# Performance work log

Measured on AMD Instinct MI355X. Metric: run time of the kernel, lower is better.

Reference implementation:

```python
import jax, jax.numpy as jnp
import numpy as np

L, B, D = 1024, 4, 1024
E, K, H = 8, 2, 4096


def setup_inputs() -> dict:
    key = jax.random.key(0)
    ks = jax.random.split(key, 12)
    s_g = 1.0 / np.sqrt(D)
    s_h = 1.0 / np.sqrt(H)
    return {
        "inputs": jax.random.normal(ks[0], (L, B, D), jnp.float32),
        "task_param": jax.random.normal(ks[1], (B, D), jnp.float32),
        "gate_img_w": jax.random.normal(ks[2], (D, E), jnp.float32) * s_g,
        "gate_img_b": jnp.zeros((E,), jnp.float32),
        "gate_txt_w": jax.random.normal(ks[3], (D, E), jnp.float32) * s_g,
        "gate_txt_b": jnp.zeros((E,), jnp.float32),
        "task_gate_w": jax.random.normal(ks[4], (D, E), jnp.float32) * s_g,
        "task_gate_b": jnp.zeros((E,), jnp.float32),
        "alpha": jnp.float32(0.5),
        "w1": jax.random.normal(ks[5], (E, D, H), jnp.float32) * s_g,
        "w2": jax.random.normal(ks[6], (E, H, D), jnp.float32) * s_h,
        "is_text": 1,
    }


def reference(inputs, task_param, gate_img_w, gate_img_b, gate_txt_w, gate_txt_b,
              task_gate_w, task_gate_b, alpha, w1, w2, is_text):
    # task gate: (B, E) -> broadcast over L
    task_logits = (task_param @ task_gate_w + task_gate_b)[None]  # (1, B, E)
    if is_text:
        input_logits = inputs @ gate_txt_w + gate_txt_b  # (L, B, E)
    else:
        input_logits = inputs @ gate_img_w + gate_img_b
    gate_logits = (1.0 - alpha) * input_logits + alpha * task_logits  # (L, B, E)

    topk_vals, sel = jax.lax.top_k(gate_logits, K)  # (L, B, K)

    # auxiliary load-balancing loss
    soft = jax.nn.softmax(gate_logits.astype(jnp.float32), axis=-1)
    avg_weight = soft.mean(axis=(0, 1))                       # (E,)
    expert_mask = jax.nn.one_hot(sel, E).sum(axis=2)          # (L, B, E)
    avg_count = expert_mask.mean(axis=(0, 1))                 # (E,)
    l_aux = jnp.mean(avg_weight * avg_count) * E

    # renormalized top-k weights, combined per expert: (L, B, E)
    weights = jax.nn.softmax(topk_vals.astype(jnp.float32), axis=-1).astype(inputs.dtype)
    comb = jnp.sum(jax.nn.one_hot(sel, E, dtype=weights.dtype) * weights[..., None], axis=2)

    # dense per-expert FFN, weighted combine (loop over fixed small E)
    results = jnp.zeros_like(inputs)
    for e in range(E):
        h = jax.nn.gelu(inputs @ w1[e])      # (L, B, H)
        out = h @ w2[e]                      # (L, B, D)
        results = results + comb[..., e:e + 1] * out
    return results, l_aux.astype(jnp.float32)
```

## Files before the change

### kernel.cpp

```cpp
#include <hip/hip_runtime.h>
#include <hip/hip_bf16.h>
#include <math.h>

#define L_ 1024
#define B_ 4
#define D_ 1024
#define E_ 8
#define K_ 2
#define H_ 4096
#define T_ (L_*B_)
#define P_ (T_*K_)
#define PPAD (P_+256)

typedef unsigned short u16;
typedef __attribute__((ext_vector_type(4))) float f32x4;
typedef __attribute__((ext_vector_type(8))) short s16x8;

__device__ __forceinline__ u16 f2bf(float f) {
  uint32_t u = __float_as_uint(f);
  uint32_t r = (u + 0x7FFFu + ((u >> 16) & 1u)) >> 16;
  return (u16)r;
}
__device__ __forceinline__ float gelu_fast(float v) {
  float u = v * (1.0f + 0.044715f * v * v);
  float t = __expf(-1.5957691216057308f * u);
  return v / (1.0f + t);
}

template<int R, int C>
__global__ void convtrans(const float* __restrict__ in, u16* __restrict__ out) {
  __shared__ float tile[64][65];
  int e = blockIdx.z;
  int r0 = blockIdx.y * 64, c0 = blockIdx.x * 64;
  const float* src = in + (size_t)e * R * C;
  u16* dst = out + (size_t)e * R * C;
  int t = threadIdx.x;
  int tr = t >> 4, tc = (t & 15) * 4;
#pragma unroll
  for (int p = 0; p < 4; ++p) {
    int r = tr + p * 16;
    float4 v = *(const float4*)(src + (size_t)(r0 + r) * C + c0 + tc);
    tile[r][tc] = v.x; tile[r][tc+1] = v.y; tile[r][tc+2] = v.z; tile[r][tc+3] = v.w;
  }
  __syncthreads();
#pragma unroll
  for (int p = 0; p < 4; ++p) {
    int c = tr + p * 16;
    ushort4 o;
    o.x = f2bf(tile[tc+0][c]); o.y = f2bf(tile[tc+1][c]);
    o.z = f2bf(tile[tc+2][c]); o.w = f2bf(tile[tc+3][c]);
    *(ushort4*)(dst + (size_t)(c0 + c) * R + r0 + tc) = o;
  }
}

__global__ void gating(const float* __restrict__ x, const float* __restrict__ task_param,
                       const float* __restrict__ gw_img, const float* __restrict__ gb_img,
                       const float* __restrict__ gw_txt, const float* __restrict__ gb_txt,
                       const float* __restrict__ tgw, const float* __restrict__ tgb,
                       const float* __restrict__ alpha_p, const int* __restrict__ is_text_p,
                       float4* __restrict__ sel_w, float* __restrict__ prob_part,
                       int* __restrict__ count_part) {
  __shared__ float wprob[4][8];
  __shared__ int wcnt[4][8];
  int wid = threadIdx.x >> 6, lane = threadIdx.x & 63;
  int t = blockIdx.x * 4 + wid;
  int b = t & (B_ - 1);
  int it = is_text_p[0];
  const float* gw = it ? gw_txt : gw_img;
  const float* gb = it ? gb_txt : gb_img;
  float alpha = alpha_p[0];
  const float* xr = x + (size_t)t * D_;
  const float* tp = task_param + (size_t)b * D_;
  float acc[8] = {0,0,0,0,0,0,0,0};
  float tac[8] = {0,0,0,0,0,0,0,0};
  for (int i = 0; i < D_/64; ++i) {
    int d = i * 64 + lane;
    float xv = xr[d], tv = tp[d];
#pragma unroll
    for (int e = 0; e < 8; ++e) {
      acc[e] += xv * gw[d*8 + e];
      tac[e] += tv * tgw[d*8 + e];
    }
  }
#pragma unroll
  for (int e = 0; e < 8; ++e) {
#pragma unroll
    for (int off = 32; off > 0; off >>= 1) {
      acc[e] += __shfl_xor(acc[e], off);
      tac[e] += __shfl_xor(tac[e], off);
    }
  }
  float lg[8];
#pragma unroll
  for (int e = 0; e < 8; ++e)
    lg[e] = (1.0f - alpha) * (acc[e] + gb[e]) + alpha * (tac[e] + tgb[e]);
  float m = lg[0];
#pragma unroll
  for (int e = 1; e < 8; ++e) m = fmaxf(m, lg[e]);
  float pr[8], ps = 0.f;
#pragma unroll
  for (int e = 0; e < 8; ++e) { pr[e] = expf(lg[e] - m); ps += pr[e]; }
  float inv = 1.0f / ps;
  int i0 = 0; float v0 = lg[0];
#pragma unroll
  for (int e = 1; e < 8; ++e) if (lg[e] > v0) { v0 = lg[e]; i0 = e; }
  int i1 = -1; float v1 = -1e30f;
#pragma unroll
  for (int e = 0; e < 8; ++e) if (e != i0 && lg[e] > v1) { v1 = lg[e]; i1 = e; }
  float ex = expf(v1 - v0);
  float w0 = 1.0f / (1.0f + ex), w1 = ex / (1.0f + ex);
  if (lane == 0) {
    sel_w[t] = make_float4(__int_as_float(i0), __int_as_float(i1), w0, w1);
#pragma unroll
    for (int e = 0; e < 8; ++e) {
      wprob[wid][e] = pr[e] * inv;
      wcnt[wid][e] = (i0 == e) + (i1 == e);
    }
  }
  __syncthreads();
  if (threadIdx.x < 8) {
    int e = threadIdx.x;
    prob_part[blockIdx.x * 8 + e] = wprob[0][e] + wprob[1][e] + wprob[2][e] + wprob[3][e];
    count_part[blockIdx.x * 8 + e] = wcnt[0][e] + wcnt[1][e] + wcnt[2][e] + wcnt[3][e];
  }
}

__global__ void finalize(const float* __restrict__ prob_part, const int* __restrict__ count_part,
                         int* __restrict__ counts, int* __restrict__ offs,
                         int* __restrict__ cursors, float* __restrict__ laux_out) {
  __shared__ float ps_[256];
  __shared__ int cs_[256];
  int t = threadIdx.x;
  int e = t & 7, s = t >> 3;
  float p = 0.f; int c = 0;
  for (int b = s; b < 1024; b += 32) { p += prob_part[b*8 + e]; c += count_part[b*8 + e]; }
  ps_[t] = p; cs_[t] = c;
  __syncthreads();
  for (int st = 16; st > 0; st >>= 1) {
    if (s < st) { ps_[t] += ps_[t + st*8]; cs_[t] += cs_[t + st*8]; }
    __syncthreads();
  }
  if (t == 0) {
    int off = 0; float laux = 0.f;
    for (int ee = 0; ee < 8; ++ee) {
      int cnt = cs_[ee];
      counts[ee] = cnt; offs[ee] = off; cursors[ee] = off; off += cnt;
      laux += (ps_[ee] * (1.0f/4096.0f)) * ((float)cnt * (1.0f/4096.0f));
    }
    *laux_out = laux;
  }
}

__global__ void scatter_gather(const float* __restrict__ x, const float4* __restrict__ sel_w,
                               int* __restrict__ cursors, float* __restrict__ pair_w,
                               int* __restrict__ pair_idx, u16* __restrict__ Xg) {
  int wid = threadIdx.x >> 6, lane = threadIdx.x & 63;
  int t = blockIdx.x * 4 + wid;
  float4 sw = sel_w[t];
  int s0 = __float_as_int(sw.x), s1 = __float_as_int(sw.y);
  int p0 = 0, p1 = 0;
  if (lane == 0) {
    p0 = atomicAdd(&cursors[s0], 1);
    p1 = atomicAdd(&cursors[s1], 1);
  }
  p0 = __shfl(p0, 0); p1 = __shfl(p1, 0);
  if (lane == 0) {
    pair_w[p0] = sw.z; pair_w[p1] = sw.w;
    pair_idx[t*2] = p0; pair_idx[t*2+1] = p1;
  }
  const float* xr = x + (size_t)t * D_;
  u16* d0 = Xg + (size_t)p0 * D_;
  u16* d1 = Xg + (size_t)p1 * D_;
#pragma unroll
  for (int i = 0; i < 4; ++i) {
    int c = i * 256 + lane * 4;
    float4 v = *(const float4*)(xr + c);
    ushort4 o;
    o.x = f2bf(v.x); o.y = f2bf(v.y); o.z = f2bf(v.z); o.w = f2bf(v.w);
    *(ushort4*)(d0 + c) = o;
    *(ushort4*)(d1 + c) = o;
  }
}

template<int EPI, int KDIM, int KLEN, int NOUT, int NPANEL, int KSPLIT, int JSLOTS>
__global__ __launch_bounds__(512, 2)
void gemm256(const u16* __restrict__ Tok, const u16* __restrict__ Wt,
             const int* __restrict__ counts, const int* __restrict__ offs,
             const float* __restrict__ pair_w,
             u16* __restrict__ Hout, float* __restrict__ Cout) {
  int gid = blockIdx.x;
  int e = gid & 7;
  int idx = gid >> 3;
  int panel = idx % NPANEL; idx /= NPANEL;
  int ks = idx % KSPLIT;    idx /= KSPLIT;
  int j0 = idx;
  int ne = counts[e];
  int off = offs[e];
  int kbase = ks * KLEN;
  float* Cpart = Cout + (size_t)ks * P_ * D_;

  __shared__ u16 As[2][16384];
  __shared__ u16 Bs[2][16384];
  int t = threadIdx.x, lane = t & 63, wid = t >> 6;
  int wf = wid & 1, wt = wid >> 1;

  const u16* Wg = Wt + (size_t)e * NOUT * KDIM + (size_t)panel * 256 * KDIM + kbase;

  int rowoff[4]; int ldsoff[4];
#pragma unroll
  for (int i = 0; i < 4; ++i) {
    int slot = i * 512 + t;
    int row = slot >> 3;
    int kk = (slot & 7) ^ (row & 7);
    rowoff[i] = row * KDIM + kk * 8;
    ldsoff[i] = slot * 8;
  }

  int aoff[8][2], boff[4][2];
#pragma unroll
  for (int r = 0; r < 8; ++r) {
    int row = wf * 128 + r * 16 + (lane & 15);
#pragma unroll
    for (int h = 0; h < 2; ++h) {
      int kk = h * 4 + (lane >> 4);
      aoff[r][h] = (row * 8 + (kk ^ (row & 7))) * 8;
    }
  }
#pragma unroll
  for (int f = 0; f < 4; ++f) {
    int row = wt * 64 + f * 16 + (lane & 15);
#pragma unroll
    for (int h = 0; h < 2; ++h) {
      int kk = h * 4 + (lane >> 4);
      boff[f][h] = (row * 8 + (kk ^ (row & 7))) * 8;
    }
  }

  constexpr int NT = KLEN / 64;
  int lr = lane & 15, lg4 = (lane >> 4) * 4;

  for (int bx = j0; bx * 256 < ne; bx += JSLOTS) {
    const u16* Tg = Tok + (size_t)(off + bx * 256) * KDIM + kbase;
    f32x4 acc[8][4] = {};
#pragma unroll
    for (int i = 0; i < 4; ++i) {
      __builtin_amdgcn_global_load_lds(
          (const __attribute__((address_space(1))) void*)(Wg + rowoff[i]),
          (__attribute__((address_space(3))) void*)(&As[0][ldsoff[i]]), 16, 0, 0);
      __builtin_amdgcn_global_load_lds(
          (const __attribute__((address_space(1))) void*)(Tg + rowoff[i]),
          (__attribute__((address_space(3))) void*)(&Bs[0][ldsoff[i]]), 16, 0, 0);
    }
    __syncthreads();
    int cur = 0;
    for (int tt = 0; tt < NT; ++tt) {
      if (tt + 1 < NT) {
        int k0 = (tt + 1) * 64;
        int nb = cur ^ 1;
#pragma unroll
        for (int i = 0; i < 4; ++i) {
          __builtin_amdgcn_global_load_lds(
              (const __attribute__((address_space(1))) void*)(Wg + rowoff[i] + k0),
              (__attribute__((address_space(3))) void*)(&As[nb][ldsoff[i]]), 16, 0, 0);
          __builtin_amdgcn_global_load_lds(
              (const __attribute__((address_space(1))) void*)(Tg + rowoff[i] + k0),
              (__attribute__((address_space(3))) void*)(&Bs[nb][ldsoff[i]]), 16, 0, 0);
        }
      }
      const u16* Ab = &As[cur][0]; const u16* Bb = &Bs[cur][0];
#pragma unroll
      for (int h = 0; h < 2; ++h) {
        s16x8 a[8], b[4];
#pragma unroll
        for (int r = 0; r < 8; ++r) a[r] = *(const s16x8*)(Ab + aoff[r][h]);
#pragma unroll
        for (int f = 0; f < 4; ++f) b[f] = *(const s16x8*)(Bb + boff[f][h]);
#pragma unroll
        for (int r = 0; r < 8; ++r)
#pragma unroll
          for (int f = 0; f < 4; ++f)
            acc[r][f] = __builtin_amdgcn_mfma_f32_16x16x32_bf16(a[r], b[f], acc[r][f], 0, 0, 0);
      }
      __syncthreads();
      cur ^= 1;
    }

#pragma unroll
    for (int f = 0; f < 4; ++f) {
      int tokl = bx * 256 + wt * 64 + f * 16 + lr;
      if (tokl >= ne) continue;
      size_t grow = (size_t)(off + tokl);
      if (EPI == 0) {
#pragma unroll
        for (int r = 0; r < 8; ++r) {
          ushort4 o;
          o.x = f2bf(gelu_fast(acc[r][f][0]));
          o.y = f2bf(gelu_fast(acc[r][f][1]));
          o.z = f2bf(gelu_fast(acc[r][f][2]));
          o.w = f2bf(gelu_fast(acc[r][f][3]));
          *(ushort4*)(Hout + grow * NOUT + panel * 256 + wf * 128 + r * 16 + lg4) = o;
        }
      } else {
        float w = pair_w[grow];
#pragma unroll
        for (int r = 0; r < 8; ++r) {
          float4 o;
          o.x = acc[r][f][0] * w; o.y = acc[r][f][1] * w;
          o.z = acc[r][f][2] * w; o.w = acc[r][f][3] * w;
          *(float4*)(Cpart + grow * NOUT + panel * 256 + wf * 128 + r * 16 + lg4) = o;
        }
      }
    }
  }
}

__global__ void combine(const float* __restrict__ pair_out, const int* __restrict__ pair_idx,
                        float* __restrict__ out) {
  const float* part1 = pair_out + (size_t)P_ * D_;
  int t = blockIdx.x;
  int p0 = pair_idx[t*2], p1 = pair_idx[t*2+1];
  int c = threadIdx.x * 4;
  float4 a0 = *(const float4*)(pair_out + (size_t)p0 * D_ + c);
  float4 a1 = *(const float4*)(part1    + (size_t)p0 * D_ + c);
  float4 b0 = *(const float4*)(pair_out + (size_t)p1 * D_ + c);
  float4 b1 = *(const float4*)(part1    + (size_t)p1 * D_ + c);
  float4 o;
  o.x = (a0.x + a1.x) + (b0.x + b1.x);
  o.y = (a0.y + a1.y) + (b0.y + b1.y);
  o.z = (a0.z + a1.z) + (b0.z + b1.z);
  o.w = (a0.w + a1.w) + (b0.w + b1.w);
  *(float4*)(out + (size_t)t * D_ + c) = o;
}

extern "C" void kernel_launch(void* const* d_in, const int* in_sizes, int n_in,
                              void* d_out, int out_size, void* d_ws, size_t ws_size,
                              hipStream_t stream) {
  const float* inputs      = (const float*)d_in[0];
  const float* task_param  = (const float*)d_in[1];
  const float* gate_img_w  = (const float*)d_in[2];
  const float* gate_img_b  = (const float*)d_in[3];
  const float* gate_txt_w  = (const float*)d_in[4];
  const float* gate_txt_b  = (const float*)d_in[5];
  const float* task_gate_w = (const float*)d_in[6];
  const float* task_gate_b = (const float*)d_in[7];
  const float* alpha       = (const float*)d_in[8];
  const float* w1          = (const float*)d_in[9];
  const float* w2          = (const float*)d_in[10];
  const int*   is_text     = (const int*)d_in[11];
  float* out = (float*)d_out;

  char* ws = (char*)d_ws;
  u16* w1b = (u16*)(ws + 0);
  u16* w2b = (u16*)(ws + 67108864);
  u16* Xg  = (u16*)(ws + 134217728);
  u16* Hb  = (u16*)(ws + 151519232);
  float4* sel_w   = (float4*)(ws + 220725248);
  float* pair_w   = (float*)(ws + 220725248 + 65536);
  int* pair_idx   = (int*)(ws + 220725248 + 98816);
  float* prob_part= (float*)(ws + 220725248 + 131584);
  int* count_part = (int*)(ws + 220725248 + 164352);
  int* counters   = (int*)(ws + 220725248 + 197120);
  float* pair_out = (float*)(ws + 0);

  int* counts  = counters;
  int* offs    = counters + 8;
  int* cursors = counters + 16;

  convtrans<D_, H_><<<dim3(H_/64, D_/64, E_), 256, 0, stream>>>(w1, w1b);
  convtrans<H_, D_><<<dim3(D_/64, H_/64, E_), 256, 0, stream>>>(w2, w2b);
  gating<<<dim3(T_/4), 256, 0, stream>>>(inputs, task_param, gate_img_w, gate_img_b,
      gate_txt_w, gate_txt_b, task_gate_w, task_gate_b, alpha, is_text,
      sel_w, prob_part, count_part);
  finalize<<<dim3(1), 256, 0, stream>>>(prob_part, count_part, counts, offs, cursors,
      out + (size_t)T_ * D_);
  scatter_gather<<<dim3(T_/4), 256, 0, stream>>>(inputs, sel_w, cursors, pair_w, pair_idx, Xg);
  gemm256<0, D_, D_, H_, 16, 1, 2><<<dim3(256), 512, 0, stream>>>(
      Xg, w1b, counts, offs, pair_w, Hb, (float*)nullptr);
  gemm256<1, H_, H_/2, D_, 4, 2, 4><<<dim3(256), 512, 0, stream>>>(
      Hb, w2b, counts, offs, pair_w, (u16*)nullptr, pair_out);
  combine<<<dim3(T_), 256, 0, stream>>>(pair_out, pair_idx, out);
}
```

Baseline: 512.5 us.

## Schedule grouped expert GEMM tiles through an atomic work queue

Replaces the fixed static mapping of blocks to (expert, panel, k-split, token-block) with a persistent work queue. The finalize kernel precomputes per-expert tile counts and prefix offsets, and each block pulls the next tile index with an atomic ticket counter. This is meant to balance uneven expert loads across the 256 blocks, so that no block idles while others loop over heavy experts. In exchange it adds an atomic and a barrier per tile plus a linear search for the expert.

```diff
diff --git a/kernel.cpp b/kernel.cpp
--- a/kernel.cpp
+++ b/kernel.cpp
@@ -26,6 +26,7 @@
   float t = __expf(-1.5957691216057308f * u);
   return v / (1.0f + t);
 }
+
 
 template<int R, int C>
 __global__ void convtrans(const float* __restrict__ in, u16* __restrict__ out) {
@@ -126,8 +127,7 @@
 }
 
 __global__ void finalize(const float* __restrict__ prob_part, const int* __restrict__ count_part,
-                         int* __restrict__ counts, int* __restrict__ offs,
-                         int* __restrict__ cursors, float* __restrict__ laux_out) {
+                         int* __restrict__ meta, float* __restrict__ laux_out) {
   __shared__ float ps_[256];
   __shared__ int cs_[256];
   int t = threadIdx.x;
@@ -142,11 +142,25 @@
   }
   if (t == 0) {
     int off = 0; float laux = 0.f;
+    int u1 = 0, u2 = 0;
     for (int ee = 0; ee < 8; ++ee) {
       int cnt = cs_[ee];
-      counts[ee] = cnt; offs[ee] = off; cursors[ee] = off; off += cnt;
+      meta[ee] = cnt;
+      meta[8 + ee] = off;
+      meta[16 + ee] = off;
+      int nb = (cnt + 255) >> 8;
+      meta[24 + ee] = nb;
+      meta[32 + ee] = u1;
+      meta[41 + ee] = u2;
+      u1 += 16 * nb;
+      u2 += 4 * nb * 2;
+      off += cnt;
       laux += (ps_[ee] * (1.0f/4096.0f)) * ((float)cnt * (1.0f/4096.0f));
     }
+    meta[32 + 8] = u1;
+    meta[41 + 8] = u2;
+    meta[50] = 0;
+    meta[51] = 0;
     *laux_out = laux;
   }
 }
@@ -182,38 +196,30 @@
   }
 }
 
-template<int EPI, int KDIM, int KLEN, int NOUT, int NPANEL, int KSPLIT, int JSLOTS>
+template<int EPI, int KDIM, int KLEN, int NOUT, int NPANEL, int KSPLIT>
 __global__ __launch_bounds__(512, 2)
 void gemm256(const u16* __restrict__ Tok, const u16* __restrict__ Wt,
-             const int* __restrict__ counts, const int* __restrict__ offs,
-             const float* __restrict__ pair_w,
+             int* __restrict__ meta, const float* __restrict__ pair_w,
              u16* __restrict__ Hout, float* __restrict__ Cout) {
-  int gid = blockIdx.x;
-  int e = gid & 7;
-  int idx = gid >> 3;
-  int panel = idx % NPANEL; idx /= NPANEL;
-  int ks = idx % KSPLIT;    idx /= KSPLIT;
-  int j0 = idx;
-  int ne = counts[e];
-  int off = offs[e];
-  int kbase = ks * KLEN;
-  float* Cpart = Cout + (size_t)ks * P_ * D_;
+  const int* offs = meta + 8;
+  const int* nbx  = meta + 24;
+  const int* ub   = (EPI == 0) ? meta + 32 : meta + 41;
+  int* tick       = meta + ((EPI == 0) ? 50 : 51);
 
   __shared__ u16 As[2][16384];
   __shared__ u16 Bs[2][16384];
+  __shared__ int s_u;
   int t = threadIdx.x, lane = t & 63, wid = t >> 6;
   int wf = wid & 1, wt = wid >> 1;
 
-  const u16* Wg = Wt + (size_t)e * NOUT * KDIM + (size_t)panel * 256 * KDIM + kbase;
-
-  int rowoff[4]; int ldsoff[4];
+  int goff[4]; int ldso[4];
 #pragma unroll
   for (int i = 0; i < 4; ++i) {
     int slot = i * 512 + t;
     int row = slot >> 3;
     int kk = (slot & 7) ^ (row & 7);
-    rowoff[i] = row * KDIM + kk * 8;
-    ldsoff[i] = slot * 8;
+    goff[i] = row * KDIM + kk * 8;
+    ldso[i] = slot * 8;
   }
 
   int aoff[8][2], boff[4][2];
@@ -238,33 +244,52 @@
 
   constexpr int NT = KLEN / 64;
   int lr = lane & 15, lg4 = (lane >> 4) * 4;
-
-  for (int bx = j0; bx * 256 < ne; bx += JSLOTS) {
+  int Utot = ub[8];
+
+  for (;;) {
+    if (t == 0) s_u = atomicAdd(tick, 1);
+    __syncthreads();
+    int u = s_u;
+    if (u >= Utot) break;
+    int e = 0;
+    while (u >= ub[e + 1]) ++e;
+    int ul = u - ub[e];
+    int nb = nbx[e];
+    int panel = ul / (nb * KSPLIT);
+    int rem   = ul - panel * (nb * KSPLIT);
+    int bx    = rem / KSPLIT;
+    int ks    = rem - bx * KSPLIT;
+    int ne  = meta[e];
+    int off = offs[e];
+    int kbase = ks * KLEN;
+    float* Cpart = Cout + (size_t)ks * P_ * D_;
+    const u16* Wg = Wt + (size_t)e * NOUT * KDIM + (size_t)panel * 256 * KDIM + kbase;
     const u16* Tg = Tok + (size_t)(off + bx * 256) * KDIM + kbase;
+
     f32x4 acc[8][4] = {};
 #pragma unroll
     for (int i = 0; i < 4; ++i) {
       __builtin_amdgcn_global_load_lds(
-          (const __attribute__((address_space(1))) void*)(Wg + rowoff[i]),
-          (__attribute__((address_space(3))) void*)(&As[0][ldsoff[i]]), 16, 0, 0);
+          (const __attribute__((address_space(1))) void*)(Wg + goff[i]),
+          (__attribute__((address_space(3))) void*)(&As[0][ldso[i]]), 16, 0, 0);
       __builtin_amdgcn_global_load_lds(
-          (const __attribute__((address_space(1))) void*)(Tg + rowoff[i]),
-          (__attribute__((address_space(3))) void*)(&Bs[0][ldsoff[i]]), 16, 0, 0);
+          (const __attribute__((address_space(1))) void*)(Tg + goff[i]),
+          (__attribute__((address_space(3))) void*)(&Bs[0][ldso[i]]), 16, 0, 0);
     }
     __syncthreads();
     int cur = 0;
     for (int tt = 0; tt < NT; ++tt) {
       if (tt + 1 < NT) {
         int k0 = (tt + 1) * 64;
-        int nb = cur ^ 1;
+        int nbuf = cur ^ 1;
 #pragma unroll
         for (int i = 0; i < 4; ++i) {
           __builtin_amdgcn_global_load_lds(
-              (const __attribute__((address_space(1))) void*)(Wg + rowoff[i] + k0),
-              (__attribute__((address_space(3))) void*)(&As[nb][ldsoff[i]]), 16, 0, 0);
+              (const __attribute__((address_space(1))) void*)(Wg + goff[i] + k0),
+              (__attribute__((address_space(3))) void*)(&As[nbuf][ldso[i]]), 16, 0, 0);
           __builtin_amdgcn_global_load_lds(
-              (const __attribute__((address_space(1))) void*)(Tg + rowoff[i] + k0),
-              (__attribute__((address_space(3))) void*)(&Bs[nb][ldsoff[i]]), 16, 0, 0);
+              (const __attribute__((address_space(1))) void*)(Tg + goff[i] + k0),
+              (__attribute__((address_space(3))) void*)(&Bs[nbuf][ldso[i]]), 16, 0, 0);
         }
       }
       const u16* Ab = &As[cur][0]; const u16* Bb = &Bs[cur][0];
@@ -359,24 +384,20 @@
   int* pair_idx   = (int*)(ws + 220725248 + 98816);
   float* prob_part= (float*)(ws + 220725248 + 131584);
   int* count_part = (int*)(ws + 220725248 + 164352);
-  int* counters   = (int*)(ws + 220725248 + 197120);
+  int* meta       = (int*)(ws + 220725248 + 197120);
   float* pair_out = (float*)(ws + 0);
-
-  int* counts  = counters;
-  int* offs    = counters + 8;
-  int* cursors = counters + 16;
 
   convtrans<D_, H_><<<dim3(H_/64, D_/64, E_), 256, 0, stream>>>(w1, w1b);
   convtrans<H_, D_><<<dim3(D_/64, H_/64, E_), 256, 0, stream>>>(w2, w2b);
   gating<<<dim3(T_/4), 256, 0, stream>>>(inputs, task_param, gate_img_w, gate_img_b,
       gate_txt_w, gate_txt_b, task_gate_w, task_gate_b, alpha, is_text,
       sel_w, prob_part, count_part);
-  finalize<<<dim3(1), 256, 0, stream>>>(prob_part, count_part, counts, offs, cursors,
+  finalize<<<dim3(1), 256, 0, stream>>>(prob_part, count_part, meta,
       out + (size_t)T_ * D_);
-  scatter_gather<<<dim3(T_/4), 256, 0, stream>>>(inputs, sel_w, cursors, pair_w, pair_idx, Xg);
-  gemm256<0, D_, D_, H_, 16, 1, 2><<<dim3(256), 512, 0, stream>>>(
-      Xg, w1b, counts, offs, pair_w, Hb, (float*)nullptr);
-  gemm256<1, H_, H_/2, D_, 4, 2, 4><<<dim3(256), 512, 0, stream>>>(
-      Hb, w2b, counts, offs, pair_w, (u16*)nullptr, pair_out);
+  scatter_gather<<<dim3(T_/4), 256, 0, stream>>>(inputs, sel_w, meta + 16, pair_w, pair_idx, Xg);
+  gemm256<0, D_, D_, H_, 16, 1><<<dim3(256), 512, 0, stream>>>(
+      Xg, w1b, meta, pair_w, Hb, (float*)nullptr);
+  gemm256<1, H_, H_/2, D_, 4, 2><<<dim3(256), 512, 0, stream>>>(
+      Hb, w2b, meta, pair_w, (u16*)nullptr, pair_out);
   combine<<<dim3(T_), 256, 0, stream>>>(pair_out, pair_idx, out);
 }
```

Result: faster. 477.8 us (-6.8%).
